# Performance work log

Hardware: AMD Instinct MI355X
Metric: run time of the kernel (lower is better)

Reference implementation:

```python
import jax, jax.numpy as jnp
import numpy as np

KEY_DIM = 32
D = 128  # attn_ratio * key_dim
H = 8
DIM = 512
N = 1024
B = 16
EPS = 1e-5


def setup_inputs() -> dict:
    key = jax.random.key(0)
    ks = jax.random.split(key, 5)
    x = jax.random.normal(ks[0], (B, DIM, N), dtype=jnp.float32)
    # grouped Conv1d(dim -> H*(2*key_dim+d), k=1, groups=H): per-group weight [H, 192, 64]
    qkv_w = jax.random.normal(ks[1], (H, 2 * KEY_DIM + D, DIM // H), dtype=jnp.float32) * 0.05
    qkv_b = jax.random.normal(ks[2], (H, 2 * KEY_DIM + D), dtype=jnp.float32) * 0.02
    # proj Conv1d(d*H -> dim, k=1)
    proj_w = jax.random.normal(ks[3], (DIM, D * H), dtype=jnp.float32) * 0.03
    proj_b = jax.random.normal(ks[4], (DIM,), dtype=jnp.float32) * 0.02
    bn_gamma = jnp.ones((DIM,), dtype=jnp.float32)
    bn_beta = jnp.zeros((DIM,), dtype=jnp.float32)
    bn_mean = jnp.zeros((DIM,), dtype=jnp.float32)
    bn_var = jnp.ones((DIM,), dtype=jnp.float32)
    return {"x": x, "qkv_w": qkv_w, "qkv_b": qkv_b, "proj_w": proj_w,
            "proj_b": proj_b, "bn_gamma": bn_gamma, "bn_beta": bn_beta,
            "bn_mean": bn_mean, "bn_var": bn_var}


def reference(x, qkv_w, qkv_b, proj_w, proj_b, bn_gamma, bn_beta, bn_mean, bn_var):
    Bx, C, Nx = x.shape
    scale = KEY_DIM ** (-0.5)
    # grouped 1x1 conv: split channels into H groups of C//H
    xh = x.reshape(Bx, H, C // H, Nx)                      # [B,H,Cg,N]
    qkv = jnp.einsum('bhcn,hoc->bhon', xh, qkv_w) + qkv_b[None, :, :, None]
    q, k, v = jnp.split(qkv, [KEY_DIM, 2 * KEY_DIM], axis=2)  # [B,H,kd,N],[B,H,kd,N],[B,H,d,N]
    # attn[m,n] = sum_c q[c,m]*k[c,n]
    attn = jnp.einsum('bhcm,bhcn->bhmn', q, k) * scale      # [B,H,N,N]
    attn = jax.nn.softmax(attn, axis=-1)
    # out[d,m] = sum_n v[d,n]*attn[m,n]  (v @ attn^T)
    o = jnp.einsum('bhdn,bhmn->bhdm', v, attn)              # [B,H,d,N]
    o = o.reshape(Bx, H * D, Nx)
    # proj: ReLU -> 1x1 conv -> BatchNorm1d (inference mode)
    o = jax.nn.relu(o)
    o = jnp.einsum('bcn,oc->bon', o, proj_w) + proj_b[None, :, None]
    inv = bn_gamma / jnp.sqrt(bn_var + EPS)
    o = o * inv[None, :, None] + (bn_beta - bn_mean * inv)[None, :, None]
    return o
```

## Files before the change

kernel.cpp:

```cpp
#include <hip/hip_runtime.h>
#include <math.h>

typedef unsigned short u16;
typedef unsigned int u32;

#define Bb   16
#define Hh   8
#define KD   32
#define DV   128
#define DIM  512
#define Nn   1024
#define OQKV 192
#define SCALE2 0.25503490221320355f

typedef short bf16x8 __attribute__((ext_vector_type(8)));
typedef float f32x16 __attribute__((ext_vector_type(16)));

#define MFMA32(a, b, c) __builtin_amdgcn_mfma_f32_32x32x16_bf16(a, b, c, 0, 0, 0)

__device__ __forceinline__ float fexp2(float x) {
#if __has_builtin(__builtin_amdgcn_exp2f)
  return __builtin_amdgcn_exp2f(x);
#else
  return exp2f(x);
#endif
}

__device__ __forceinline__ u16 f2bf_rn(float f) {
  return (u16)((__float_as_uint(f) + 0x8000u) >> 16);
}

#if __has_builtin(__builtin_amdgcn_cvt_pk_bf16_f32)
__device__ __forceinline__ u32 pk2(float lo, float hi) {
  auto r = __builtin_amdgcn_cvt_pk_bf16_f32(lo, hi);
  return __builtin_bit_cast(u32, r);
}
#else
__device__ __forceinline__ u32 pk2(float lo, float hi) {
  u32 a = __float_as_uint(lo) + 0x8000u;
  u32 b = __float_as_uint(hi) + 0x8000u;
  return __builtin_amdgcn_perm(b, a, 0x07060302);
}
#endif

#if __has_builtin(__builtin_amdgcn_permlane32_swap)
__device__ __forceinline__ void pswap(u32& a, u32& b) {
  auto r = __builtin_amdgcn_permlane32_swap(a, b, false, false);
  a = r[0]; b = r[1];
}
#else
__device__ __forceinline__ void pswap(u32& a, u32& b) {
  asm("v_permlane32_swap_b32 %0, %1" : "+v"(a), "+v"(b));
}
#endif

__device__ __forceinline__ uint4 cvt8(const float* __restrict__ src) {
  float4 a = *(const float4*)src;
  float4 b = *(const float4*)(src + 4);
  uint4 r;
  r.x = pk2(a.x, a.y); r.y = pk2(a.z, a.w);
  r.z = pk2(b.x, b.y); r.w = pk2(b.z, b.w);
  return r;
}

__global__ __launch_bounds__(256) void qkv_kernel(
    const float* __restrict__ x, const float* __restrict__ qw,
    const float* __restrict__ bias, u16* __restrict__ Qb,
    u16* __restrict__ Kb, u16* __restrict__ Vb) {
  const int nt = blockIdx.x, bh = blockIdx.y;
  const int b = bh >> 3, h = bh & 7;
  const int tid = threadIdx.x;
  const int wid = tid >> 6, lane = tid & 63;
  const int r32 = lane & 31, hh = lane >> 5;
  const int n0 = nt * 128;

  __shared__ __align__(16) union SH {
    struct { u16 Ws[192 * 72]; u16 Xs[128 * 72]; } s;
    u16 Vt[128 * 136];
  } sh;

  const float* wqp = qw + (size_t)h * OQKV * 64;
  #pragma unroll
  for (int i = 0; i < 6; ++i) {
    int idx = i * 256 + tid;
    int o = idx >> 3, c8 = (idx & 7) * 8;
    *(uint4*)&sh.s.Ws[o * 72 + c8] = cvt8(&wqp[o * 64 + c8]);
  }
  const float* xp = x + ((size_t)b * DIM + h * 64) * Nn + n0;
  #pragma unroll
  for (int i = 0; i < 4; ++i) {
    int idx = i * 256 + tid;
    int cp = idx >> 5, n4 = (idx & 31) * 4;
    const int c = 2 * cp;
    float4 a = *(const float4*)&xp[(size_t)c * Nn + n4];
    float4 d = *(const float4*)&xp[(size_t)(c + 1) * Nn + n4];
    *(u32*)&sh.s.Xs[(n4 + 0) * 72 + c] = pk2(a.x, d.x);
    *(u32*)&sh.s.Xs[(n4 + 1) * 72 + c] = pk2(a.y, d.y);
    *(u32*)&sh.s.Xs[(n4 + 2) * 72 + c] = pk2(a.z, d.z);
    *(u32*)&sh.s.Xs[(n4 + 3) * 72 + c] = pk2(a.w, d.w);
  }
  __syncthreads();

  f32x16 acc[6];
  #pragma unroll
  for (int t = 0; t < 6; ++t)
    #pragma unroll
    for (int r = 0; r < 16; ++r) acc[t][r] = 0.0f;

  const int nw = wid * 32;
  #pragma unroll
  for (int k = 0; k < 4; ++k) {
    const int ko = k * 16 + hh * 8;
    bf16x8 xb = *(const bf16x8*)&sh.s.Xs[(nw + r32) * 72 + ko];
    #pragma unroll
    for (int t = 0; t < 6; ++t) {
      bf16x8 wa = *(const bf16x8*)&sh.s.Ws[(t * 32 + r32) * 72 + ko];
      acc[t] = MFMA32(wa, xb, acc[t]);
    }
  }

  __syncthreads();

  const int nl = nw + r32;
  const int n = n0 + nl;
  const float* bp = bias + h * OQKV;
  #pragma unroll
  for (int t = 0; t < 6; ++t) {
    #pragma unroll
    for (int g = 0; g < 4; ++g) {
      const int ob = t * 32 + 8 * g + 4 * hh;
      float4 bv = *(const float4*)&bp[ob];
      float v0 = acc[t][4 * g + 0] + bv.x;
      float v1 = acc[t][4 * g + 1] + bv.y;
      float v2 = acc[t][4 * g + 2] + bv.z;
      float v3 = acc[t][4 * g + 3] + bv.w;
      if (t == 0) {
        uint2 pk;
        pk.x = pk2(v0 * SCALE2, v1 * SCALE2);
        pk.y = pk2(v2 * SCALE2, v3 * SCALE2);
        *(uint2*)&Qb[((size_t)bh * Nn + n) * 32 + ob] = pk;
      } else if (t == 1) {
        uint2 pk; pk.x = pk2(v0, v1); pk.y = pk2(v2, v3);
        *(uint2*)&Kb[((size_t)bh * Nn + n) * 32 + ob - 32] = pk;
      } else {
        const int d = ob - 64;
        sh.Vt[(d + 0) * 136 + nl] = f2bf_rn(v0);
        sh.Vt[(d + 1) * 136 + nl] = f2bf_rn(v1);
        sh.Vt[(d + 2) * 136 + nl] = f2bf_rn(v2);
        sh.Vt[(d + 3) * 136 + nl] = f2bf_rn(v3);
      }
    }
  }
  __syncthreads();

  const int dd0 = tid >> 4;
  const int nn = (tid & 15) * 8;
  #pragma unroll
  for (int i = 0; i < 8; ++i) {
    const int dd = dd0 + i * 16;
    uint4 vv = *(const uint4*)&sh.Vt[dd * 136 + nn];
    *(uint4*)&Vb[((size_t)bh * DV + dd) * Nn + n0 + nn] = vv;
  }
}

__global__ __launch_bounds__(256) void attn_kernel(
    const u16* __restrict__ Qb, const u16* __restrict__ Kb,
    const u16* __restrict__ Vb, u16* __restrict__ Ot) {
  const int blk = blockIdx.x;
  const int xcd = blk & 7, j = blk >> 3;
  const int bh = (xcd << 4) | (j >> 3);
  const int mt = j & 7;
  const int tid = threadIdx.x;
  const int wid = tid >> 6, lane = tid & 63;
  const int r32 = lane & 31, hh = lane >> 5;
  const int mw = mt * 128 + wid * 32;

  __shared__ __align__(16) u16 Vs[2][128 * 72];

  const u16* qp = Qb + ((size_t)bh * Nn + mw + r32) * 32;
  const bf16x8 qb0 = *(const bf16x8*)&qp[hh * 8];
  const bf16x8 qb1 = *(const bf16x8*)&qp[16 + hh * 8];

  const u16* kbase = Kb + (size_t)bh * Nn * 32;
  const u16* vbase = Vb + (size_t)bh * DV * Nn;

  int sd[4], sn[4];
  #pragma unroll
  for (int i = 0; i < 4; ++i) {
    int idx = i * 256 + tid;
    sd[i] = idx >> 3; sn[i] = (idx & 7) * 8;
  }

  uint4 vreg[4];
  #pragma unroll
  for (int i = 0; i < 4; ++i)
    vreg[i] = *(const uint4*)&vbase[(size_t)sd[i] * Nn + sn[i]];
  #pragma unroll
  for (int i = 0; i < 4; ++i)
    *(uint4*)&Vs[0][sd[i] * 72 + sn[i]] = vreg[i];

  bf16x8 ka[4], kb[4];
  {
    const u16* kp0 = kbase + (size_t)r32 * 32;
    const u16* kp1 = kbase + (size_t)(32 + r32) * 32;
    ka[0] = *(const bf16x8*)&kp0[hh * 8];
    ka[1] = *(const bf16x8*)&kp0[16 + hh * 8];
    ka[2] = *(const bf16x8*)&kp1[hh * 8];
    ka[3] = *(const bf16x8*)&kp1[16 + hh * 8];
  }
  f32x16 c0, c1;
  #pragma unroll
  for (int r = 0; r < 16; ++r) { c0[r] = 0.0f; c1[r] = 0.0f; }
  c0 = MFMA32(ka[0], qb0, c0);
  c0 = MFMA32(ka[1], qb1, c0);
  c1 = MFMA32(ka[2], qb0, c1);
  c1 = MFMA32(ka[3], qb1, c1);

  {
    const u16* kp0 = kbase + (size_t)(64 + r32) * 32;
    const u16* kp1 = kbase + (size_t)(96 + r32) * 32;
    ka[0] = *(const bf16x8*)&kp0[hh * 8];
    ka[1] = *(const bf16x8*)&kp0[16 + hh * 8];
    ka[2] = *(const bf16x8*)&kp1[hh * 8];
    ka[3] = *(const bf16x8*)&kp1[16 + hh * 8];
  }

  f32x16 o[4];
  #pragma unroll
  for (int t = 0; t < 4; ++t)
    #pragma unroll
    for (int r = 0; r < 16; ++r) o[t][r] = 0.0f;
  float lsum = 0.0f;
  u32 Pk[16];
  union { u32 d[4]; bf16x8 v; } pbf[4];

  auto finishS = [&]() {
    float csum = 0.0f;
    #pragma unroll
    for (int r = 0; r < 16; ++r) { c0[r] = fexp2(c0[r]); csum += c0[r]; }
    #pragma unroll
    for (int r = 0; r < 16; ++r) { c1[r] = fexp2(c1[r]); csum += c1[r]; }
    lsum += csum;
    #pragma unroll
    for (int g = 0; g < 4; ++g) {
      Pk[2 * g]     = pk2(c0[4 * g + 0], c0[4 * g + 1]);
      Pk[2 * g + 1] = pk2(c0[4 * g + 2], c0[4 * g + 3]);
      Pk[8 + 2 * g]     = pk2(c1[4 * g + 0], c1[4 * g + 1]);
      Pk[8 + 2 * g + 1] = pk2(c1[4 * g + 2], c1[4 * g + 3]);
    }
    pswap(Pk[0], Pk[2]);   pswap(Pk[1], Pk[3]);
    pswap(Pk[4], Pk[6]);   pswap(Pk[5], Pk[7]);
    pswap(Pk[8], Pk[10]);  pswap(Pk[9], Pk[11]);
    pswap(Pk[12], Pk[14]); pswap(Pk[13], Pk[15]);
    #pragma unroll
    for (int i = 0; i < 4; ++i) {
      pbf[i].d[0] = Pk[4 * i + 0];
      pbf[i].d[1] = Pk[4 * i + 1];
      pbf[i].d[2] = Pk[4 * i + 2];
      pbf[i].d[3] = Pk[4 * i + 3];
    }
  };

  finishS();

  auto iter = [&](int ch, bf16x8 (&kin)[4], bf16x8 (&kout)[4]) {
    const int p = ch & 1;
    __syncthreads();

    #pragma unroll
    for (int i = 0; i < 4; ++i)
      vreg[i] = *(const uint4*)&vbase[(size_t)sd[i] * Nn + (ch + 1) * 64 + sn[i]];

    __builtin_amdgcn_s_setprio(1);
    #pragma unroll
    for (int r = 0; r < 16; ++r) { c0[r] = 0.0f; c1[r] = 0.0f; }
    c0 = MFMA32(kin[0], qb0, c0);
    c0 = MFMA32(kin[1], qb1, c0);
    c1 = MFMA32(kin[2], qb0, c1);
    c1 = MFMA32(kin[3], qb1, c1);

    {
      const u16* kp0 = kbase + (size_t)((ch + 2) * 64 + r32) * 32;
      const u16* kp1 = kbase + (size_t)((ch + 2) * 64 + 32 + r32) * 32;
      kout[0] = *(const bf16x8*)&kp0[hh * 8];
      kout[1] = *(const bf16x8*)&kp0[16 + hh * 8];
      kout[2] = *(const bf16x8*)&kp1[hh * 8];
      kout[3] = *(const bf16x8*)&kp1[16 + hh * 8];
    }

    #pragma unroll
    for (int t = 0; t < 4; ++t) {
      const u16* vrow = &Vs[p][(t * 32 + r32) * 72];
      #pragma unroll
      for (int s = 0; s < 4; ++s) {
        bf16x8 va = *(const bf16x8*)&vrow[s * 16 + hh * 8];
        o[t] = MFMA32(va, pbf[s].v, o[t]);
      }
    }
    __builtin_amdgcn_s_setprio(0);

    #pragma unroll
    for (int i = 0; i < 4; ++i)
      *(uint4*)&Vs[1 - p][sd[i] * 72 + sn[i]] = vreg[i];

    finishS();
  };

  for (int pr = 0; pr < 7; ++pr) {
    iter(2 * pr, ka, kb);
    iter(2 * pr + 1, kb, ka);
  }
  iter(14, ka, kb);

  __syncthreads();
  __builtin_amdgcn_s_setprio(1);
  #pragma unroll
  for (int t = 0; t < 4; ++t) {
    const u16* vrow = &Vs[1][(t * 32 + r32) * 72];
    #pragma unroll
    for (int s = 0; s < 4; ++s) {
      bf16x8 va = *(const bf16x8*)&vrow[s * 16 + hh * 8];
      o[t] = MFMA32(va, pbf[s].v, o[t]);
    }
  }
  __builtin_amdgcn_s_setprio(0);

  lsum += __shfl_xor(lsum, 32, 64);
  const float inv = 1.0f / lsum;
  const int m = mw + r32;
  const int b = bh >> 3, h = bh & 7;
  u16* obase = Ot + ((size_t)b * Nn + m) * 1024 + h * DV + 4 * hh;
  #pragma unroll
  for (int t = 0; t < 4; ++t) {
    #pragma unroll
    for (int g = 0; g < 4; ++g) {
      float v0 = fmaxf(o[t][4 * g + 0] * inv, 0.0f);
      float v1 = fmaxf(o[t][4 * g + 1] * inv, 0.0f);
      float v2 = fmaxf(o[t][4 * g + 2] * inv, 0.0f);
      float v3 = fmaxf(o[t][4 * g + 3] * inv, 0.0f);
      uint2 pk; pk.x = pk2(v0, v1); pk.y = pk2(v2, v3);
      *(uint2*)&obase[t * 32 + 8 * g] = pk;
    }
  }
}

__global__ __launch_bounds__(256) void proj_kernel(
    const u16* __restrict__ Ot, const float* __restrict__ pw,
    const float* __restrict__ pb, const float* __restrict__ g,
    const float* __restrict__ bt, const float* __restrict__ mn,
    const float* __restrict__ vr, float* __restrict__ out) {
  const int blk = blockIdx.x;
  const int xcd = blk & 7, rr = blk >> 3;
  const int pairl = rr >> 2, oct = rr & 3;
  const int pair = xcd * 16 + pairl;
  const int b = pair >> 3, nt = pair & 7;
  const int n0 = nt * 128, oc0 = oct * 128;
  const int tid = threadIdx.x;
  const int wid = tid >> 6, lane = tid & 63;
  const int r32 = lane & 31, hh = lane >> 5;
  const int ocw = (wid >> 1) * 64, nw = (wid & 1) * 64;

  __shared__ __align__(16) u16 Ws[128 * 72];
  __shared__ __align__(16) u16 Os[128 * 72];
  __shared__ __align__(16) float invL[128];
  __shared__ __align__(16) float addL[128];

  if (tid < 128) {
    const int oc = oc0 + tid;
    float inv = g[oc] * rsqrtf(vr[oc] + 1e-5f);
    invL[tid] = inv;
    addL[tid] = pb[oc] * inv + bt[oc] - mn[oc] * inv;
  }

  f32x16 o[2][2];
  #pragma unroll
  for (int t = 0; t < 2; ++t)
    #pragma unroll
    for (int u = 0; u < 2; ++u)
      #pragma unroll
      for (int r = 0; r < 16; ++r) o[t][u][r] = 0.0f;

  for (int ic0 = 0; ic0 < 1024; ic0 += 64) {
    __syncthreads();
    #pragma unroll
    for (int i = 0; i < 4; ++i) {
      int idx = i * 256 + tid;
      int row = idx >> 3, c8 = (idx & 7) * 8;
      *(uint4*)&Ws[row * 72 + c8] =
          cvt8(&pw[(size_t)(oc0 + row) * 1024 + ic0 + c8]);
    }
    #pragma unroll
    for (int i = 0; i < 4; ++i) {
      int idx = i * 256 + tid;
      int row = idx >> 3, c8 = (idx & 7) * 8;
      *(uint4*)&Os[row * 72 + c8] =
          *(const uint4*)&Ot[((size_t)b * Nn + n0 + row) * 1024 + ic0 + c8];
    }
    __syncthreads();

    #pragma unroll
    for (int s = 0; s < 4; ++s) {
      const int ko = s * 16 + hh * 8;
      bf16x8 a0 = *(const bf16x8*)&Ws[(ocw + r32) * 72 + ko];
      bf16x8 a1 = *(const bf16x8*)&Ws[(ocw + 32 + r32) * 72 + ko];
      bf16x8 b0 = *(const bf16x8*)&Os[(nw + r32) * 72 + ko];
      bf16x8 b1 = *(const bf16x8*)&Os[(nw + 32 + r32) * 72 + ko];
      o[0][0] = MFMA32(a0, b0, o[0][0]);
      o[0][1] = MFMA32(a0, b1, o[0][1]);
      o[1][0] = MFMA32(a1, b0, o[1][0]);
      o[1][1] = MFMA32(a1, b1, o[1][1]);
    }
  }

  #pragma unroll
  for (int t = 0; t < 2; ++t) {
    const int lbase = ocw + t * 32 + 4 * hh;
    #pragma unroll
    for (int g = 0; g < 4; ++g) {
      const int l = lbase + 8 * g;
      const int oc = oc0 + l;
      float4 iv = *(const float4*)&invL[l];
      float4 av = *(const float4*)&addL[l];
      #pragma unroll
      for (int u = 0; u < 2; ++u) {
        const int n = n0 + nw + u * 32 + r32;
        out[((size_t)b * DIM + oc + 0) * Nn + n] = o[t][u][4 * g + 0] * iv.x + av.x;
        out[((size_t)b * DIM + oc + 1) * Nn + n] = o[t][u][4 * g + 1] * iv.y + av.y;
        out[((size_t)b * DIM + oc + 2) * Nn + n] = o[t][u][4 * g + 2] * iv.z + av.z;
        out[((size_t)b * DIM + oc + 3) * Nn + n] = o[t][u][4 * g + 3] * iv.w + av.w;
      }
    }
  }
}

extern "C" void kernel_launch(void* const* d_in, const int* in_sizes, int n_in,
                              void* d_out, int out_size, void* d_ws,
                              size_t ws_size, hipStream_t stream) {
  const float* x      = (const float*)d_in[0];
  const float* qkv_w  = (const float*)d_in[1];
  const float* qkv_b  = (const float*)d_in[2];
  const float* proj_w = (const float*)d_in[3];
  const float* proj_b = (const float*)d_in[4];
  const float* bn_g   = (const float*)d_in[5];
  const float* bn_b   = (const float*)d_in[6];
  const float* bn_m   = (const float*)d_in[7];
  const float* bn_v   = (const float*)d_in[8];
  float* out = (float*)d_out;

  char* ws = (char*)d_ws;
  u16* Qb   = (u16*)(ws);
  u16* Kb   = (u16*)(ws + 8388608);
  u16* Vb   = (u16*)(ws + 16777216);
  u16* Ot   = (u16*)(ws + 50331648);

  qkv_kernel<<<dim3(8, Bb * Hh), 256, 0, stream>>>(x, qkv_w, qkv_b, Qb, Kb, Vb);
  attn_kernel<<<dim3(1024), 256, 0, stream>>>(Qb, Kb, Vb, Ot);
  proj_kernel<<<dim3(512), 256, 0, stream>>>(Ot, proj_w, proj_b, bn_g, bn_b,
                                             bn_m, bn_v, out);
}
```

Baseline: 212.7 us.

## Load V fragments directly from global memory instead of LDS double buffer

```diff
diff --git a/kernel.cpp b/kernel.cpp
--- a/kernel.cpp
+++ b/kernel.cpp
@@ -175,31 +175,14 @@
   const int r32 = lane & 31, hh = lane >> 5;
   const int mw = mt * 128 + wid * 32;
 
-  __shared__ __align__(16) u16 Vs[2][128 * 72];
-
   const u16* qp = Qb + ((size_t)bh * Nn + mw + r32) * 32;
   const bf16x8 qb0 = *(const bf16x8*)&qp[hh * 8];
   const bf16x8 qb1 = *(const bf16x8*)&qp[16 + hh * 8];
 
   const u16* kbase = Kb + (size_t)bh * Nn * 32;
-  const u16* vbase = Vb + (size_t)bh * DV * Nn;
-
-  int sd[4], sn[4];
-  #pragma unroll
-  for (int i = 0; i < 4; ++i) {
-    int idx = i * 256 + tid;
-    sd[i] = idx >> 3; sn[i] = (idx & 7) * 8;
-  }
-
-  uint4 vreg[4];
-  #pragma unroll
-  for (int i = 0; i < 4; ++i)
-    vreg[i] = *(const uint4*)&vbase[(size_t)sd[i] * Nn + sn[i]];
-  #pragma unroll
-  for (int i = 0; i < 4; ++i)
-    *(uint4*)&Vs[0][sd[i] * 72 + sn[i]] = vreg[i];
-
-  bf16x8 ka[4], kb[4];
+  const u16* vb = Vb + (size_t)bh * DV * Nn + (size_t)r32 * Nn + hh * 8;
+
+  bf16x8 ka[4];
   {
     const u16* kp0 = kbase + (size_t)r32 * 32;
     const u16* kp1 = kbase + (size_t)(32 + r32) * 32;
@@ -263,65 +246,53 @@
 
   finishS();
 
-  auto iter = [&](int ch, bf16x8 (&kin)[4], bf16x8 (&kout)[4]) {
-    const int p = ch & 1;
-    __syncthreads();
-
-    #pragma unroll
-    for (int i = 0; i < 4; ++i)
-      vreg[i] = *(const uint4*)&vbase[(size_t)sd[i] * Nn + (ch + 1) * 64 + sn[i]];
-
+  for (int ch = 0; ch < 15; ++ch) {
     __builtin_amdgcn_s_setprio(1);
     #pragma unroll
     for (int r = 0; r < 16; ++r) { c0[r] = 0.0f; c1[r] = 0.0f; }
-    c0 = MFMA32(kin[0], qb0, c0);
-    c0 = MFMA32(kin[1], qb1, c0);
-    c1 = MFMA32(kin[2], qb0, c1);
-    c1 = MFMA32(kin[3], qb1, c1);
+    c0 = MFMA32(ka[0], qb0, c0);
+    c0 = MFMA32(ka[1], qb1, c0);
+    c1 = MFMA32(ka[2], qb0, c1);
+    c1 = MFMA32(ka[3], qb1, c1);
+
+    #pragma unroll
+    for (int t = 0; t < 4; ++t) {
+      const u16* vrow = vb + (size_t)(t * 32) * Nn + ch * 64;
+      bf16x8 v0 = *(const bf16x8*)&vrow[0];
+      bf16x8 v1 = *(const bf16x8*)&vrow[16];
+      bf16x8 v2 = *(const bf16x8*)&vrow[32];
+      bf16x8 v3 = *(const bf16x8*)&vrow[48];
+      o[t] = MFMA32(v0, pbf[0].v, o[t]);
+      o[t] = MFMA32(v1, pbf[1].v, o[t]);
+      o[t] = MFMA32(v2, pbf[2].v, o[t]);
+      o[t] = MFMA32(v3, pbf[3].v, o[t]);
+    }
+    __builtin_amdgcn_s_setprio(0);
 
     {
       const u16* kp0 = kbase + (size_t)((ch + 2) * 64 + r32) * 32;
       const u16* kp1 = kbase + (size_t)((ch + 2) * 64 + 32 + r32) * 32;
-      kout[0] = *(const bf16x8*)&kp0[hh * 8];
-      kout[1] = *(const bf16x8*)&kp0[16 + hh * 8];
-      kout[2] = *(const bf16x8*)&kp1[hh * 8];
-      kout[3] = *(const bf16x8*)&kp1[16 + hh * 8];
-    }
-
-    #pragma unroll
-    for (int t = 0; t < 4; ++t) {
-      const u16* vrow = &Vs[p][(t * 32 + r32) * 72];
-      #pragma unroll
-      for (int s = 0; s < 4; ++s) {
-        bf16x8 va = *(const bf16x8*)&vrow[s * 16 + hh * 8];
-        o[t] = MFMA32(va, pbf[s].v, o[t]);
-      }
-    }
-    __builtin_amdgcn_s_setprio(0);
-
-    #pragma unroll
-    for (int i = 0; i < 4; ++i)
-      *(uint4*)&Vs[1 - p][sd[i] * 72 + sn[i]] = vreg[i];
+      ka[0] = *(const bf16x8*)&kp0[hh * 8];
+      ka[1] = *(const bf16x8*)&kp0[16 + hh * 8];
+      ka[2] = *(const bf16x8*)&kp1[hh * 8];
+      ka[3] = *(const bf16x8*)&kp1[16 + hh * 8];
+    }
 
     finishS();
-  };
-
-  for (int pr = 0; pr < 7; ++pr) {
-    iter(2 * pr, ka, kb);
-    iter(2 * pr + 1, kb, ka);
-  }
-  iter(14, ka, kb);
-
-  __syncthreads();
+  }
+
   __builtin_amdgcn_s_setprio(1);
   #pragma unroll
   for (int t = 0; t < 4; ++t) {
-    const u16* vrow = &Vs[1][(t * 32 + r32) * 72];
-    #pragma unroll
-    for (int s = 0; s < 4; ++s) {
-      bf16x8 va = *(const bf16x8*)&vrow[s * 16 + hh * 8];
-      o[t] = MFMA32(va, pbf[s].v, o[t]);
-    }
+    const u16* vrow = vb + (size_t)(t * 32) * Nn + 15 * 64;
+    bf16x8 v0 = *(const bf16x8*)&vrow[0];
+    bf16x8 v1 = *(const bf16x8*)&vrow[16];
+    bf16x8 v2 = *(const bf16x8*)&vrow[32];
+    bf16x8 v3 = *(const bf16x8*)&vrow[48];
+    o[t] = MFMA32(v0, pbf[0].v, o[t]);
+    o[t] = MFMA32(v1, pbf[1].v, o[t]);
+    o[t] = MFMA32(v2, pbf[2].v, o[t]);
+    o[t] = MFMA32(v3, pbf[3].v, o[t]);
   }
   __builtin_amdgcn_s_setprio(0);
 
```

Measured after the change: 299.8 us. +41.0%, slower.

## Stage Q/K through shared memory for coalesced stores; simplify attention K prefetch loop

Applied to the files above, without the earlier changes.

```diff
diff --git a/kernel.cpp b/kernel.cpp
--- a/kernel.cpp
+++ b/kernel.cpp
@@ -76,7 +76,7 @@
 
   __shared__ __align__(16) union SH {
     struct { u16 Ws[192 * 72]; u16 Xs[128 * 72]; } s;
-    u16 Vt[128 * 136];
+    struct { u16 Vt[128 * 136]; u16 Qs[128 * 32]; u16 Ks[128 * 32]; } o;
   } sh;
 
   const float* wqp = qw + (size_t)h * OQKV * 64;
@@ -122,7 +122,6 @@
   __syncthreads();
 
   const int nl = nw + r32;
-  const int n = n0 + nl;
   const float* bp = bias + h * OQKV;
   #pragma unroll
   for (int t = 0; t < 6; ++t) {
@@ -138,16 +137,16 @@
         uint2 pk;
         pk.x = pk2(v0 * SCALE2, v1 * SCALE2);
         pk.y = pk2(v2 * SCALE2, v3 * SCALE2);
-        *(uint2*)&Qb[((size_t)bh * Nn + n) * 32 + ob] = pk;
+        *(uint2*)&sh.o.Qs[nl * 32 + ob] = pk;
       } else if (t == 1) {
         uint2 pk; pk.x = pk2(v0, v1); pk.y = pk2(v2, v3);
-        *(uint2*)&Kb[((size_t)bh * Nn + n) * 32 + ob - 32] = pk;
+        *(uint2*)&sh.o.Ks[nl * 32 + ob - 32] = pk;
       } else {
         const int d = ob - 64;
-        sh.Vt[(d + 0) * 136 + nl] = f2bf_rn(v0);
-        sh.Vt[(d + 1) * 136 + nl] = f2bf_rn(v1);
-        sh.Vt[(d + 2) * 136 + nl] = f2bf_rn(v2);
-        sh.Vt[(d + 3) * 136 + nl] = f2bf_rn(v3);
+        sh.o.Vt[(d + 0) * 136 + nl] = f2bf_rn(v0);
+        sh.o.Vt[(d + 1) * 136 + nl] = f2bf_rn(v1);
+        sh.o.Vt[(d + 2) * 136 + nl] = f2bf_rn(v2);
+        sh.o.Vt[(d + 3) * 136 + nl] = f2bf_rn(v3);
       }
     }
   }
@@ -158,8 +157,19 @@
   #pragma unroll
   for (int i = 0; i < 8; ++i) {
     const int dd = dd0 + i * 16;
-    uint4 vv = *(const uint4*)&sh.Vt[dd * 136 + nn];
+    uint4 vv = *(const uint4*)&sh.o.Vt[dd * 136 + nn];
     *(uint4*)&Vb[((size_t)bh * DV + dd) * Nn + n0 + nn] = vv;
+  }
+  {
+    const size_t base = ((size_t)bh * Nn + n0) * 32;
+    uint4 q0 = *(const uint4*)&sh.o.Qs[tid * 16];
+    uint4 q1 = *(const uint4*)&sh.o.Qs[tid * 16 + 8];
+    *(uint4*)&Qb[base + tid * 16] = q0;
+    *(uint4*)&Qb[base + tid * 16 + 8] = q1;
+    uint4 k0 = *(const uint4*)&sh.o.Ks[tid * 16];
+    uint4 k1 = *(const uint4*)&sh.o.Ks[tid * 16 + 8];
+    *(uint4*)&Kb[base + tid * 16] = k0;
+    *(uint4*)&Kb[base + tid * 16 + 8] = k1;
   }
 }
 
@@ -199,7 +209,7 @@
   for (int i = 0; i < 4; ++i)
     *(uint4*)&Vs[0][sd[i] * 72 + sn[i]] = vreg[i];
 
-  bf16x8 ka[4], kb[4];
+  bf16x8 ka[4];
   {
     const u16* kp0 = kbase + (size_t)r32 * 32;
     const u16* kp1 = kbase + (size_t)(32 + r32) * 32;
@@ -263,7 +273,7 @@
 
   finishS();
 
-  auto iter = [&](int ch, bf16x8 (&kin)[4], bf16x8 (&kout)[4]) {
+  for (int ch = 0; ch < 15; ++ch) {
     const int p = ch & 1;
     __syncthreads();
 
@@ -274,18 +284,19 @@
     __builtin_amdgcn_s_setprio(1);
     #pragma unroll
     for (int r = 0; r < 16; ++r) { c0[r] = 0.0f; c1[r] = 0.0f; }
-    c0 = MFMA32(kin[0], qb0, c0);
-    c0 = MFMA32(kin[1], qb1, c0);
-    c1 = MFMA32(kin[2], qb0, c1);
-    c1 = MFMA32(kin[3], qb1, c1);
-
+    c0 = MFMA32(ka[0], qb0, c0);
+    c0 = MFMA32(ka[1], qb1, c0);
+    c1 = MFMA32(ka[2], qb0, c1);
+    c1 = MFMA32(ka[3], qb1, c1);
+
+    bf16x8 kn[4];
     {
       const u16* kp0 = kbase + (size_t)((ch + 2) * 64 + r32) * 32;
       const u16* kp1 = kbase + (size_t)((ch + 2) * 64 + 32 + r32) * 32;
-      kout[0] = *(const bf16x8*)&kp0[hh * 8];
-      kout[1] = *(const bf16x8*)&kp0[16 + hh * 8];
-      kout[2] = *(const bf16x8*)&kp1[hh * 8];
-      kout[3] = *(const bf16x8*)&kp1[16 + hh * 8];
+      kn[0] = *(const bf16x8*)&kp0[hh * 8];
+      kn[1] = *(const bf16x8*)&kp0[16 + hh * 8];
+      kn[2] = *(const bf16x8*)&kp1[hh * 8];
+      kn[3] = *(const bf16x8*)&kp1[16 + hh * 8];
     }
 
     #pragma unroll
@@ -304,13 +315,10 @@
       *(uint4*)&Vs[1 - p][sd[i] * 72 + sn[i]] = vreg[i];
 
     finishS();
-  };
-
-  for (int pr = 0; pr < 7; ++pr) {
-    iter(2 * pr, ka, kb);
-    iter(2 * pr + 1, kb, ka);
-  }
-  iter(14, ka, kb);
+
+    #pragma unroll
+    for (int i = 0; i < 4; ++i) ka[i] = kn[i];
+  }
 
   __syncthreads();
   __builtin_amdgcn_s_setprio(1);
```

New measurement: 189.1 us. -11.1%, faster.
